# Optimization experiments

Measured on AMD Instinct MI355X. Metric: run time of the kernel, lower is better.

Reference implementation:

```python
import jax, jax.numpy as jnp
import numpy as np

N_NODES = 10000
NEG_SLOPE = 0.2
EPS = 1e-16


def gat_layer(x, W, a_src, a_dst, bias, src, dst):
    # x: [N, Fin], W: [Fin, Fout], a_src/a_dst: [Fout], bias: [Fout]
    h = x @ W                                  # [N, Fout]
    al_s = h @ a_src                           # [N]
    al_d = h @ a_dst                           # [N]
    e = jax.nn.leaky_relu(al_s[src] + al_d[dst], NEG_SLOPE)   # [E]
    # segment softmax over edges grouped by destination node
    m = jax.ops.segment_max(e, dst, num_segments=N_NODES)     # [N]
    ex = jnp.exp(e - m[dst])
    s = jax.ops.segment_sum(ex, dst, num_segments=N_NODES)    # [N]
    alpha = ex / (s[dst] + EPS)                                # [E]
    out = jax.ops.segment_sum(h[src] * alpha[:, None], dst, num_segments=N_NODES)
    return out + bias


def add_self_loops(edge_index):
    loop = jnp.arange(N_NODES, dtype=edge_index.dtype)
    return jnp.concatenate([edge_index, jnp.stack([loop, loop])], axis=1)


def setup_inputs() -> dict:
    key = jax.random.key(0)
    ks = jax.random.split(key, 12)
    F_in, F_hid, F_out = 256, 256, 256
    x = jax.random.normal(ks[0], (N_NODES, F_in), dtype=jnp.float32)
    pos_edge_index = jax.random.randint(ks[1], (2, 320000), 0, N_NODES)
    edge_index = jax.random.randint(ks[2], (2, 100000), 0, N_NODES)
    sc = lambda f: 1.0 / np.sqrt(f)
    Win_W = jax.random.normal(ks[3], (F_in, F_in), dtype=jnp.float32) * sc(F_in)
    Win_b = jnp.zeros((F_in,), dtype=jnp.float32)
    W1 = jax.random.normal(ks[4], (F_in, F_hid), dtype=jnp.float32) * sc(F_in)
    a1_src = jax.random.normal(ks[5], (F_hid,), dtype=jnp.float32) * sc(F_hid)
    a1_dst = jax.random.normal(ks[6], (F_hid,), dtype=jnp.float32) * sc(F_hid)
    b1 = jnp.zeros((F_hid,), dtype=jnp.float32)
    W2 = jax.random.normal(ks[7], (F_hid, F_out), dtype=jnp.float32) * sc(F_hid)
    a2_src = jax.random.normal(ks[8], (F_out,), dtype=jnp.float32) * sc(F_out)
    a2_dst = jax.random.normal(ks[9], (F_out,), dtype=jnp.float32) * sc(F_out)
    b2 = jnp.zeros((F_out,), dtype=jnp.float32)
    return {
        "x": x, "pos_edge_index": pos_edge_index, "edge_index": edge_index,
        "Win_W": Win_W, "Win_b": Win_b,
        "W1": W1, "a1_src": a1_src, "a1_dst": a1_dst, "b1": b1,
        "W2": W2, "a2_src": a2_src, "a2_dst": a2_dst, "b2": b2,
    }


def reference(x, pos_edge_index, edge_index, Win_W, Win_b,
              W1, a1_src, a1_dst, b1, W2, a2_src, a2_dst, b2):
    ei = add_self_loops(pos_edge_index)
    src, dst = ei[0], ei[1]
    h = x @ Win_W + Win_b                       # input_weighting Linear
    h = gat_layer(h, W1, a1_src, a1_dst, b1, src, dst)
    h = gat_layer(h, W2, a2_src, a2_dst, b2, src, dst)
    logits = jnp.sum(h[edge_index[0]] * h[edge_index[1]], axis=-1)
    return logits
```

## Files before the change

### kernel.cpp

```cpp
#include <hip/hip_runtime.h>
#include <math.h>

#define FDIM 256
#define NEG_SLOPE 0.2f

typedef _Float16 half4v __attribute__((ext_vector_type(4)));
typedef _Float16 half8v __attribute__((ext_vector_type(8)));
typedef float f32x4 __attribute__((ext_vector_type(4)));


__global__ void hist_dst(const int* __restrict__ pos_ei, int* __restrict__ cnt,
                         int E_pos, int E_tot) {
    int e = blockIdx.x * blockDim.x + threadIdx.x;
    if (e < E_tot) {
        int d = (e < E_pos) ? pos_ei[E_pos + e] : (e - E_pos);
        atomicAdd(&cnt[d], 1);
    }
}

__global__ __launch_bounds__(1024) void scan10k(const int* __restrict__ cnt,
                                                int* __restrict__ row_ptr,
                                                int* __restrict__ fill, int N) {
    const int CH = 10;
    __shared__ int sums[1024];
    int tid = threadIdx.x;
    int base = tid * CH;
    int vals[CH];
    int s = 0;
#pragma unroll
    for (int i = 0; i < CH; ++i) {
        int idx = base + i;
        int v = (idx < N) ? cnt[idx] : 0;
        vals[i] = s;
        s += v;
    }
    sums[tid] = s;
    __syncthreads();
    for (int off = 1; off < 1024; off <<= 1) {
        int v = (tid >= off) ? sums[tid - off] : 0;
        __syncthreads();
        sums[tid] += v;
        __syncthreads();
    }
    int toff = (tid == 0) ? 0 : sums[tid - 1];
#pragma unroll
    for (int i = 0; i < CH; ++i) {
        int idx = base + i;
        if (idx < N) {
            int rp = toff + vals[i];
            row_ptr[idx] = rp;
            fill[idx] = rp;
        }
    }
    if (tid == 0) row_ptr[N] = sums[1023];
}

__global__ void scatter_edges(const int* __restrict__ pos_ei, int* __restrict__ fill,
                              int* __restrict__ srcs, int E_pos, int E_tot) {
    int e = blockIdx.x * blockDim.x + threadIdx.x;
    if (e < E_tot) {
        int s, d;
        if (e < E_pos) { s = pos_ei[e]; d = pos_ei[E_pos + e]; }
        else           { s = e - E_pos; d = s; }
        int pos = atomicAdd(&fill[d], 1);
        srcs[pos] = s;
    }
}


__global__ __launch_bounds__(256) void prep_weights(const float* __restrict__ W0,
                                                    const float* __restrict__ W1,
                                                    const float* __restrict__ W2,
                                                    _Float16* __restrict__ Wt_hi,
                                                    _Float16* __restrict__ Wt_lo) {
    int n = blockIdx.x;
    int mat = blockIdx.y;
    const float* W = (mat == 0) ? W0 : (mat == 1) ? W1 : W2;
    int k = threadIdx.x;
    float v = W[k * FDIM + n];
    _Float16 hi = (_Float16)v;
    _Float16 lo = (_Float16)(v - (float)hi);
    size_t o = (size_t)mat * FDIM * FDIM + (size_t)n * FDIM + k;
    Wt_hi[o] = hi;
    Wt_lo[o] = lo;
}


template <int MODE>
__global__ __launch_bounds__(256) void gemm_mfma(
        const float* __restrict__ A32,
        const _Float16* __restrict__ A_hi, const _Float16* __restrict__ A_lo,
        const _Float16* __restrict__ Bt_hi, const _Float16* __restrict__ Bt_lo,
        const float* __restrict__ bias,
        const float* __restrict__ a_src, const float* __restrict__ a_dst,
        float* __restrict__ al_s, float* __restrict__ al_d,
        _Float16* __restrict__ C_hi, _Float16* __restrict__ C_lo,
        int M) {
    __shared__ _Float16 As_hi[64][72];
    __shared__ _Float16 As_lo[64][72];
    __shared__ _Float16 Bs_hi[64][72];
    __shared__ _Float16 Bs_lo[64][72];
    int tid = threadIdx.x;
    int lane = tid & 63, w = tid >> 6;
    int wm = w >> 1, wn = w & 1;
    int quad = lane >> 4, l16 = lane & 15;
    int mBase = blockIdx.x * 64, nBase = blockIdx.y * 64;
    f32x4 acc[2][2] = {};

    for (int k0 = 0; k0 < FDIM; k0 += 64) {
        __syncthreads();
        if (MODE == 0) {
#pragma unroll
            for (int i = 0; i < 4; ++i) {
                int f = tid + i * 256;
                int m = f >> 4, kc = (f & 15) << 2;
                int row = mBase + m;
                float4 a = make_float4(0.f, 0.f, 0.f, 0.f);
                if (row < M) a = *(const float4*)(A32 + (size_t)row * FDIM + k0 + kc);
                _Float16 hx = (_Float16)a.x, hy = (_Float16)a.y;
                _Float16 hz = (_Float16)a.z, hw = (_Float16)a.w;
                half4v hi = {hx, hy, hz, hw};
                half4v lo = {(_Float16)(a.x - (float)hx), (_Float16)(a.y - (float)hy),
                             (_Float16)(a.z - (float)hz), (_Float16)(a.w - (float)hw)};
                *(half4v*)&As_hi[m][kc] = hi;
                *(half4v*)&As_lo[m][kc] = lo;
            }
        } else {
#pragma unroll
            for (int i = 0; i < 2; ++i) {
                int g = tid + i * 256;
                int m = g >> 3, gk = (g & 7) << 3;
                int row = mBase + m;
                half8v hi, lo;
                if (row < M) {
                    size_t off = (size_t)row * FDIM + k0 + gk;
                    hi = *(const half8v*)(A_hi + off);
                    lo = *(const half8v*)(A_lo + off);
                } else {
                    _Float16 z = (_Float16)0.f;
                    hi = (half8v){z, z, z, z, z, z, z, z};
                    lo = hi;
                }
                *(half8v*)&As_hi[m][gk] = hi;
                *(half8v*)&As_lo[m][gk] = lo;
            }
        }
#pragma unroll
        for (int i = 0; i < 2; ++i) {
            int g = tid + i * 256;
            int n = g >> 3, gk = (g & 7) << 3;
            size_t off = (size_t)(nBase + n) * FDIM + k0 + gk;
            *(half8v*)&Bs_hi[n][gk] = *(const half8v*)(Bt_hi + off);
            *(half8v*)&Bs_lo[n][gk] = *(const half8v*)(Bt_lo + off);
        }
        __syncthreads();
#pragma unroll
        for (int ks = 0; ks < 2; ++ks) {
            int kcol = ks * 32 + quad * 8;
            half8v aHi[2], aLo[2], bHi[2], bLo[2];
#pragma unroll
            for (int mt = 0; mt < 2; ++mt) {
                int r = wm * 32 + mt * 16 + l16;
                aHi[mt] = *(const half8v*)&As_hi[r][kcol];
                aLo[mt] = *(const half8v*)&As_lo[r][kcol];
            }
#pragma unroll
            for (int nt = 0; nt < 2; ++nt) {
                int c = wn * 32 + nt * 16 + l16;
                bHi[nt] = *(const half8v*)&Bs_hi[c][kcol];
                bLo[nt] = *(const half8v*)&Bs_lo[c][kcol];
            }
#pragma unroll
            for (int mt = 0; mt < 2; ++mt)
#pragma unroll
                for (int nt = 0; nt < 2; ++nt) {
                    acc[mt][nt] = __builtin_amdgcn_mfma_f32_16x16x32_f16(
                        aHi[mt], bHi[nt], acc[mt][nt], 0, 0, 0);
                    acc[mt][nt] = __builtin_amdgcn_mfma_f32_16x16x32_f16(
                        aHi[mt], bLo[nt], acc[mt][nt], 0, 0, 0);
                    acc[mt][nt] = __builtin_amdgcn_mfma_f32_16x16x32_f16(
                        aLo[mt], bHi[nt], acc[mt][nt], 0, 0, 0);
                }
        }
    }

    int col0 = nBase + wn * 32 + l16;
    int col1 = col0 + 16;
    if (MODE == 0) {
        float b0 = bias[col0], b1v = bias[col1];
#pragma unroll
        for (int mt = 0; mt < 2; ++mt) {
#pragma unroll
            for (int r = 0; r < 4; ++r) {
                int row = mBase + wm * 32 + mt * 16 + quad * 4 + r;
                if (row >= M) continue;
                float o0 = acc[mt][0][r] + b0;
                float o1 = acc[mt][1][r] + b1v;
                _Float16 h0 = (_Float16)o0, h1 = (_Float16)o1;
                size_t p0 = (size_t)row * FDIM + col0;
                size_t p1 = (size_t)row * FDIM + col1;
                C_hi[p0] = h0;              C_hi[p1] = h1;
                C_lo[p0] = (_Float16)(o0 - (float)h0);
                C_lo[p1] = (_Float16)(o1 - (float)h1);
            }
        }
    } else {
        float as0 = a_src[col0], as1 = a_src[col1];
        float ad0 = a_dst[col0], ad1 = a_dst[col1];
#pragma unroll
        for (int mt = 0; mt < 2; ++mt) {
#pragma unroll
            for (int r = 0; r < 4; ++r) {
                int row = mBase + wm * 32 + mt * 16 + quad * 4 + r;
                if (row < M) {
                    C_hi[(size_t)row * FDIM + col0] = (_Float16)acc[mt][0][r];
                    C_hi[(size_t)row * FDIM + col1] = (_Float16)acc[mt][1][r];
                }
                float ps = acc[mt][0][r] * as0 + acc[mt][1][r] * as1;
                float pd = acc[mt][0][r] * ad0 + acc[mt][1][r] * ad1;
#pragma unroll
                for (int off = 8; off; off >>= 1) {
                    ps += __shfl_xor(ps, off);
                    pd += __shfl_xor(pd, off);
                }
                if (l16 == 0 && row < M) {
                    atomicAdd(&al_s[row], ps);
                    atomicAdd(&al_d[row], pd);
                }
            }
        }
    }
}


__global__ __launch_bounds__(256) void softagg(
        const _Float16* __restrict__ t, const float* __restrict__ al_s,
        const float* __restrict__ al_d, const int* __restrict__ row_ptr,
        const int* __restrict__ srcs, const float* __restrict__ bias,
        _Float16* __restrict__ out_hi, _Float16* __restrict__ out_lo,
        float* __restrict__ out32, int N) {
    int wave = threadIdx.x >> 6, lane = threadIdx.x & 63;
    int node = blockIdx.x * 4 + wave;
    if (node >= N) return;
    int beg = row_ptr[node], end = row_ptr[node + 1];
    int deg = end - beg;
    float ad = al_d[node];
    const _Float16* tb = t + (size_t)lane * 4;
    float4 acc = make_float4(0.f, 0.f, 0.f, 0.f);
    float ssum = 0.f;

    if (deg <= 256) {
        float e[4];
        int sj[4];
#pragma unroll
        for (int c = 0; c < 4; ++c) {
            e[c] = -INFINITY;
            sj[c] = 0;
            int j = beg + c * 64 + lane;
            if (j < end) {
                int s = srcs[j];
                sj[c] = s;
                float ee = al_s[s] + ad;
                e[c] = (ee > 0.f) ? ee : NEG_SLOPE * ee;
            }
        }
        float m = fmaxf(fmaxf(e[0], e[1]), fmaxf(e[2], e[3]));
#pragma unroll
        for (int o = 32; o; o >>= 1) m = fmaxf(m, __shfl_xor(m, o));
        float ex[4];
#pragma unroll
        for (int c = 0; c < 4; ++c) {
            ex[c] = (e[c] == -INFINITY) ? 0.f : __expf(e[c] - m);
            ssum += ex[c];
        }
#pragma unroll
        for (int c = 0; c < 4; ++c) {
            int jc = beg + c * 64;
            if (jc >= end) break;
            int cnt = min(64, end - jc);
            int jj = 0;
            for (; jj + 4 <= cnt; jj += 4) {
                float a0 = __shfl(ex[c], jj + 0), a1 = __shfl(ex[c], jj + 1);
                float a2 = __shfl(ex[c], jj + 2), a3 = __shfl(ex[c], jj + 3);
                int r0 = __shfl(sj[c], jj + 0), r1 = __shfl(sj[c], jj + 1);
                int r2 = __shfl(sj[c], jj + 2), r3 = __shfl(sj[c], jj + 3);
                half4v v0 = *(const half4v*)(tb + (size_t)r0 * FDIM);
                half4v v1 = *(const half4v*)(tb + (size_t)r1 * FDIM);
                half4v v2 = *(const half4v*)(tb + (size_t)r2 * FDIM);
                half4v v3 = *(const half4v*)(tb + (size_t)r3 * FDIM);
                acc.x = fmaf(a0, (float)v0.x, acc.x); acc.y = fmaf(a0, (float)v0.y, acc.y);
                acc.z = fmaf(a0, (float)v0.z, acc.z); acc.w = fmaf(a0, (float)v0.w, acc.w);
                acc.x = fmaf(a1, (float)v1.x, acc.x); acc.y = fmaf(a1, (float)v1.y, acc.y);
                acc.z = fmaf(a1, (float)v1.z, acc.z); acc.w = fmaf(a1, (float)v1.w, acc.w);
                acc.x = fmaf(a2, (float)v2.x, acc.x); acc.y = fmaf(a2, (float)v2.y, acc.y);
                acc.z = fmaf(a2, (float)v2.z, acc.z); acc.w = fmaf(a2, (float)v2.w, acc.w);
                acc.x = fmaf(a3, (float)v3.x, acc.x); acc.y = fmaf(a3, (float)v3.y, acc.y);
                acc.z = fmaf(a3, (float)v3.z, acc.z); acc.w = fmaf(a3, (float)v3.w, acc.w);
            }
            for (; jj < cnt; ++jj) {
                float a = __shfl(ex[c], jj);
                int r = __shfl(sj[c], jj);
                half4v v = *(const half4v*)(tb + (size_t)r * FDIM);
                acc.x = fmaf(a, (float)v.x, acc.x); acc.y = fmaf(a, (float)v.y, acc.y);
                acc.z = fmaf(a, (float)v.z, acc.z); acc.w = fmaf(a, (float)v.w, acc.w);
            }
        }
    } else {
        float m = -INFINITY;
        for (int j = beg + lane; j < end; j += 64) {
            float ee = al_s[srcs[j]] + ad;
            ee = (ee > 0.f) ? ee : NEG_SLOPE * ee;
            m = fmaxf(m, ee);
        }
#pragma unroll
        for (int o = 32; o; o >>= 1) m = fmaxf(m, __shfl_xor(m, o));
        for (int jc = beg; jc < end; jc += 64) {
            int j = jc + lane;
            float ex = 0.f;
            int sr = 0;
            if (j < end) {
                sr = srcs[j];
                float ee = al_s[sr] + ad;
                ee = (ee > 0.f) ? ee : NEG_SLOPE * ee;
                ex = __expf(ee - m);
                ssum += ex;
            }
            int cnt = min(64, end - jc);
            for (int jj = 0; jj < cnt; ++jj) {
                float a = __shfl(ex, jj);
                int r = __shfl(sr, jj);
                half4v v = *(const half4v*)(tb + (size_t)r * FDIM);
                acc.x = fmaf(a, (float)v.x, acc.x); acc.y = fmaf(a, (float)v.y, acc.y);
                acc.z = fmaf(a, (float)v.z, acc.z); acc.w = fmaf(a, (float)v.w, acc.w);
            }
        }
    }

#pragma unroll
    for (int o = 32; o; o >>= 1) ssum += __shfl_xor(ssum, o);
    float inv = 1.f / (ssum + 1e-16f);
    float4 bv = ((const float4*)bias)[lane];
    float ox = fmaf(acc.x, inv, bv.x);
    float oy = fmaf(acc.y, inv, bv.y);
    float oz = fmaf(acc.z, inv, bv.z);
    float ow = fmaf(acc.w, inv, bv.w);
    if (out32) {
        ((float4*)out32)[node * 64 + lane] = make_float4(ox, oy, oz, ow);
    } else {
        _Float16 hx = (_Float16)ox, hy = (_Float16)oy;
        _Float16 hz = (_Float16)oz, hw = (_Float16)ow;
        half4v hi = {hx, hy, hz, hw};
        half4v lo = {(_Float16)(ox - (float)hx), (_Float16)(oy - (float)hy),
                     (_Float16)(oz - (float)hz), (_Float16)(ow - (float)hw)};
        *(half4v*)(out_hi + (size_t)node * FDIM + lane * 4) = hi;
        *(half4v*)(out_lo + (size_t)node * FDIM + lane * 4) = lo;
    }
}


__global__ __launch_bounds__(256) void edge_dot(const float* __restrict__ h,
                                                const int* __restrict__ ei,
                                                float* __restrict__ out, int EQ) {
    int w = threadIdx.x >> 6, lane = threadIdx.x & 63;
    int e = blockIdx.x * 4 + w;
    if (e >= EQ) return;
    int u = ei[e], v = ei[EQ + e];
    const float4* hu = (const float4*)(h + (size_t)u * FDIM);
    const float4* hv = (const float4*)(h + (size_t)v * FDIM);
    float4 a = hu[lane], b = hv[lane];
    float s = a.x * b.x + a.y * b.y + a.z * b.z + a.w * b.w;
#pragma unroll
    for (int o = 32; o; o >>= 1) s += __shfl_down(s, o);
    if (lane == 0) out[e] = s;
}


extern "C" void kernel_launch(void* const* d_in, const int* in_sizes, int n_in,
                              void* d_out, int out_size, void* d_ws, size_t ws_size,
                              hipStream_t stream) {
    const float* x       = (const float*)d_in[0];
    const int*   pos_ei  = (const int*)d_in[1];
    const int*   q_ei    = (const int*)d_in[2];
    const float* Win_W   = (const float*)d_in[3];
    const float* Win_b   = (const float*)d_in[4];
    const float* W1      = (const float*)d_in[5];
    const float* a1_src  = (const float*)d_in[6];
    const float* a1_dst  = (const float*)d_in[7];
    const float* b1      = (const float*)d_in[8];
    const float* W2      = (const float*)d_in[9];
    const float* a2_src  = (const float*)d_in[10];
    const float* a2_dst  = (const float*)d_in[11];
    const float* b2      = (const float*)d_in[12];
    float* logits = (float*)d_out;

    const int N = in_sizes[0] / FDIM;
    const int E_pos = in_sizes[1] / 2;
    const int EQ = in_sizes[2] / 2;
    const int E_tot = E_pos + N;
    const size_t WMAT = (size_t)FDIM * FDIM;
    const size_t NF = (size_t)N * FDIM;

    _Float16* Wt_hi = (_Float16*)d_ws;
    _Float16* Wt_lo = Wt_hi + 3 * WMAT;
    _Float16* h0_hi = Wt_lo + 3 * WMAT;
    _Float16* h0_lo = h0_hi + NF;
    _Float16* t_h   = h0_lo + NF;
    float* h32   = (float*)(t_h + NF);
    float* al_s1 = h32 + NF;
    float* al_d1 = al_s1 + N;
    float* al_s2 = al_d1 + N;
    float* al_d2 = al_s2 + N;
    int* cnt     = (int*)(al_d2 + N);
    int* row_ptr = cnt + N;
    int* fill    = row_ptr + (N + 1);
    int* srcs    = fill + N;

    hipMemsetAsync(al_s1, 0, (size_t)(4 * N) * sizeof(float) + (size_t)N * sizeof(int), stream);

    {
        int nb = (E_tot + 255) / 256;
        hist_dst<<<nb, 256, 0, stream>>>(pos_ei, cnt, E_pos, E_tot);
        scan10k<<<1, 1024, 0, stream>>>(cnt, row_ptr, fill, N);
        scatter_edges<<<nb, 256, 0, stream>>>(pos_ei, fill, srcs, E_pos, E_tot);
    }

    prep_weights<<<dim3(FDIM, 3), 256, 0, stream>>>(Win_W, W1, W2, Wt_hi, Wt_lo);

    dim3 ggrid((N + 63) / 64, FDIM / 64);
    int nblk4 = (N + 3) / 4;

    gemm_mfma<0><<<ggrid, 256, 0, stream>>>(x, nullptr, nullptr, Wt_hi, Wt_lo, Win_b,
                                            nullptr, nullptr, nullptr, nullptr,
                                            h0_hi, h0_lo, N);

    gemm_mfma<1><<<ggrid, 256, 0, stream>>>(nullptr, h0_hi, h0_lo,
                                            Wt_hi + WMAT, Wt_lo + WMAT, nullptr,
                                            a1_src, a1_dst, al_s1, al_d1,
                                            t_h, nullptr, N);
    softagg<<<nblk4, 256, 0, stream>>>(t_h, al_s1, al_d1, row_ptr, srcs, b1,
                                       h0_hi, h0_lo, nullptr, N);

    gemm_mfma<1><<<ggrid, 256, 0, stream>>>(nullptr, h0_hi, h0_lo,
                                            Wt_hi + 2 * WMAT, Wt_lo + 2 * WMAT, nullptr,
                                            a2_src, a2_dst, al_s2, al_d2,
                                            t_h, nullptr, N);
    softagg<<<nblk4, 256, 0, stream>>>(t_h, al_s2, al_d2, row_ptr, srcs, b2,
                                       nullptr, nullptr, h32, N);

    edge_dot<<<(EQ + 3) / 4, 256, 0, stream>>>(h32, q_ei, logits, EQ);
}
```

Before: 239.3 us.

## Fuse graph-build kernels, batch softagg gathers by 8, group query edges by source

Merges the histogram and weight-prep kernels into one launch and the scatter into another, and adds a CSR build for the query edges keyed by source node. The final edge-dot kernel then walks each source's query edges so the source row is loaded once and reused. The softagg gather loops now issue 8 independent row loads per round instead of 4 or 1, to raise memory-level parallelism. The costs are an extra scan and scatter for the query CSR, and out-of-range shuffle lanes in partial rounds (their rows are still loaded but presumably weighted by zero).

```diff
diff --git a/kernel.cpp b/kernel.cpp
--- a/kernel.cpp
+++ b/kernel.cpp
@@ -9,20 +9,41 @@
 typedef float f32x4 __attribute__((ext_vector_type(4)));
 
 
-__global__ void hist_dst(const int* __restrict__ pos_ei, int* __restrict__ cnt,
-                         int E_pos, int E_tot) {
-    int e = blockIdx.x * blockDim.x + threadIdx.x;
-    if (e < E_tot) {
-        int d = (e < E_pos) ? pos_ei[E_pos + e] : (e - E_pos);
-        atomicAdd(&cnt[d], 1);
-    }
-}
-
-__global__ __launch_bounds__(1024) void scan10k(const int* __restrict__ cnt,
-                                                int* __restrict__ row_ptr,
-                                                int* __restrict__ fill, int N) {
+__global__ void build_phase1(const int* __restrict__ pos_ei, const int* __restrict__ q_ei,
+                             int* __restrict__ cnt, int* __restrict__ qcnt,
+                             const float* __restrict__ W0, const float* __restrict__ W1,
+                             const float* __restrict__ W2,
+                             _Float16* __restrict__ Wt_hi, _Float16* __restrict__ Wt_lo,
+                             int E_pos, int E_tot, int EQ, int nbE, int nbQ) {
+    int b = blockIdx.x;
+    int tid = threadIdx.x;
+    if (b < nbE) {
+        int e = b * 256 + tid;
+        if (e < E_tot) {
+            int d = (e < E_pos) ? pos_ei[E_pos + e] : (e - E_pos);
+            atomicAdd(&cnt[d], 1);
+        }
+    } else if (b < nbE + nbQ) {
+        int e = (b - nbE) * 256 + tid;
+        if (e < EQ) atomicAdd(&qcnt[q_ei[e]], 1);
+    } else {
+        int idx = b - nbE - nbQ;
+        int n = idx & 255, mat = idx >> 8;
+        const float* W = (mat == 0) ? W0 : (mat == 1) ? W1 : W2;
+        int k = tid;
+        float v = W[k * FDIM + n];
+        _Float16 hi = (_Float16)v;
+        _Float16 lo = (_Float16)(v - (float)hi);
+        size_t o = (size_t)mat * FDIM * FDIM + (size_t)n * FDIM + k;
+        Wt_hi[o] = hi;
+        Wt_lo[o] = lo;
+    }
+}
+
+
+__device__ void scan_body(const int* __restrict__ cnt, int* __restrict__ row_ptr,
+                          int* __restrict__ fill, int N, int* sums) {
     const int CH = 10;
-    __shared__ int sums[1024];
     int tid = threadIdx.x;
     int base = tid * CH;
     int vals[CH];
@@ -55,34 +76,43 @@
     if (tid == 0) row_ptr[N] = sums[1023];
 }
 
-__global__ void scatter_edges(const int* __restrict__ pos_ei, int* __restrict__ fill,
-                              int* __restrict__ srcs, int E_pos, int E_tot) {
-    int e = blockIdx.x * blockDim.x + threadIdx.x;
-    if (e < E_tot) {
-        int s, d;
-        if (e < E_pos) { s = pos_ei[e]; d = pos_ei[E_pos + e]; }
-        else           { s = e - E_pos; d = s; }
-        int pos = atomicAdd(&fill[d], 1);
-        srcs[pos] = s;
-    }
-}
-
-
-__global__ __launch_bounds__(256) void prep_weights(const float* __restrict__ W0,
-                                                    const float* __restrict__ W1,
-                                                    const float* __restrict__ W2,
-                                                    _Float16* __restrict__ Wt_hi,
-                                                    _Float16* __restrict__ Wt_lo) {
-    int n = blockIdx.x;
-    int mat = blockIdx.y;
-    const float* W = (mat == 0) ? W0 : (mat == 1) ? W1 : W2;
-    int k = threadIdx.x;
-    float v = W[k * FDIM + n];
-    _Float16 hi = (_Float16)v;
-    _Float16 lo = (_Float16)(v - (float)hi);
-    size_t o = (size_t)mat * FDIM * FDIM + (size_t)n * FDIM + k;
-    Wt_hi[o] = hi;
-    Wt_lo[o] = lo;
+__global__ __launch_bounds__(1024) void scan2(const int* __restrict__ cnt,
+                                              int* __restrict__ row_ptr, int* __restrict__ fill,
+                                              const int* __restrict__ qcnt,
+                                              int* __restrict__ qrow_ptr, int* __restrict__ qfill,
+                                              int N) {
+    __shared__ int sums[1024];
+    scan_body(cnt, row_ptr, fill, N, sums);
+    __syncthreads();
+    scan_body(qcnt, qrow_ptr, qfill, N, sums);
+}
+
+
+__global__ void build_phase2(const int* __restrict__ pos_ei, const int* __restrict__ q_ei,
+                             int* __restrict__ fill, int* __restrict__ srcs,
+                             int* __restrict__ qfill, int* __restrict__ qdst,
+                             int* __restrict__ qeid,
+                             int E_pos, int E_tot, int EQ, int nbE) {
+    int b = blockIdx.x;
+    int tid = threadIdx.x;
+    if (b < nbE) {
+        int e = b * 256 + tid;
+        if (e < E_tot) {
+            int s, d;
+            if (e < E_pos) { s = pos_ei[e]; d = pos_ei[E_pos + e]; }
+            else           { s = e - E_pos; d = s; }
+            int pos = atomicAdd(&fill[d], 1);
+            srcs[pos] = s;
+        }
+    } else {
+        int e = (b - nbE) * 256 + tid;
+        if (e < EQ) {
+            int u = q_ei[e];
+            int pos = atomicAdd(&qfill[u], 1);
+            qdst[pos] = q_ei[EQ + e];
+            qeid[pos] = e;
+        }
+    }
 }
 
 
@@ -278,31 +308,27 @@
             int jc = beg + c * 64;
             if (jc >= end) break;
             int cnt = min(64, end - jc);
-            int jj = 0;
-            for (; jj + 4 <= cnt; jj += 4) {
-                float a0 = __shfl(ex[c], jj + 0), a1 = __shfl(ex[c], jj + 1);
-                float a2 = __shfl(ex[c], jj + 2), a3 = __shfl(ex[c], jj + 3);
-                int r0 = __shfl(sj[c], jj + 0), r1 = __shfl(sj[c], jj + 1);
-                int r2 = __shfl(sj[c], jj + 2), r3 = __shfl(sj[c], jj + 3);
-                half4v v0 = *(const half4v*)(tb + (size_t)r0 * FDIM);
-                half4v v1 = *(const half4v*)(tb + (size_t)r1 * FDIM);
-                half4v v2 = *(const half4v*)(tb + (size_t)r2 * FDIM);
-                half4v v3 = *(const half4v*)(tb + (size_t)r3 * FDIM);
-                acc.x = fmaf(a0, (float)v0.x, acc.x); acc.y = fmaf(a0, (float)v0.y, acc.y);
-                acc.z = fmaf(a0, (float)v0.z, acc.z); acc.w = fmaf(a0, (float)v0.w, acc.w);
-                acc.x = fmaf(a1, (float)v1.x, acc.x); acc.y = fmaf(a1, (float)v1.y, acc.y);
-                acc.z = fmaf(a1, (float)v1.z, acc.z); acc.w = fmaf(a1, (float)v1.w, acc.w);
-                acc.x = fmaf(a2, (float)v2.x, acc.x); acc.y = fmaf(a2, (float)v2.y, acc.y);
-                acc.z = fmaf(a2, (float)v2.z, acc.z); acc.w = fmaf(a2, (float)v2.w, acc.w);
-                acc.x = fmaf(a3, (float)v3.x, acc.x); acc.y = fmaf(a3, (float)v3.y, acc.y);
-                acc.z = fmaf(a3, (float)v3.z, acc.z); acc.w = fmaf(a3, (float)v3.w, acc.w);
-            }
-            for (; jj < cnt; ++jj) {
-                float a = __shfl(ex[c], jj);
-                int r = __shfl(sj[c], jj);
-                half4v v = *(const half4v*)(tb + (size_t)r * FDIM);
-                acc.x = fmaf(a, (float)v.x, acc.x); acc.y = fmaf(a, (float)v.y, acc.y);
-                acc.z = fmaf(a, (float)v.z, acc.z); acc.w = fmaf(a, (float)v.w, acc.w);
+            int rounds = (cnt + 7) >> 3;
+            for (int g = 0; g < rounds; ++g) {
+                int jj = g * 8;
+                float av[8];
+                int rv[8];
+#pragma unroll
+                for (int q = 0; q < 8; ++q) {
+                    av[q] = __shfl(ex[c], jj + q);
+                    rv[q] = __shfl(sj[c], jj + q);
+                }
+                half4v vv[8];
+#pragma unroll
+                for (int q = 0; q < 8; ++q)
+                    vv[q] = *(const half4v*)(tb + (size_t)rv[q] * FDIM);
+#pragma unroll
+                for (int q = 0; q < 8; ++q) {
+                    acc.x = fmaf(av[q], (float)vv[q].x, acc.x);
+                    acc.y = fmaf(av[q], (float)vv[q].y, acc.y);
+                    acc.z = fmaf(av[q], (float)vv[q].z, acc.z);
+                    acc.w = fmaf(av[q], (float)vv[q].w, acc.w);
+                }
             }
         }
     } else {
@@ -326,12 +352,27 @@
                 ssum += ex;
             }
             int cnt = min(64, end - jc);
-            for (int jj = 0; jj < cnt; ++jj) {
-                float a = __shfl(ex, jj);
-                int r = __shfl(sr, jj);
-                half4v v = *(const half4v*)(tb + (size_t)r * FDIM);
-                acc.x = fmaf(a, (float)v.x, acc.x); acc.y = fmaf(a, (float)v.y, acc.y);
-                acc.z = fmaf(a, (float)v.z, acc.z); acc.w = fmaf(a, (float)v.w, acc.w);
+            int rounds = (cnt + 7) >> 3;
+            for (int g = 0; g < rounds; ++g) {
+                int jj = g * 8;
+                float av[8];
+                int rv[8];
+#pragma unroll
+                for (int q = 0; q < 8; ++q) {
+                    av[q] = __shfl(ex, jj + q);
+                    rv[q] = __shfl(sr, jj + q);
+                }
+                half4v vv[8];
+#pragma unroll
+                for (int q = 0; q < 8; ++q)
+                    vv[q] = *(const half4v*)(tb + (size_t)rv[q] * FDIM);
+#pragma unroll
+                for (int q = 0; q < 8; ++q) {
+                    acc.x = fmaf(av[q], (float)vv[q].x, acc.x);
+                    acc.y = fmaf(av[q], (float)vv[q].y, acc.y);
+                    acc.z = fmaf(av[q], (float)vv[q].z, acc.z);
+                    acc.w = fmaf(av[q], (float)vv[q].w, acc.w);
+                }
             }
         }
     }
@@ -358,20 +399,41 @@
 }
 
 
-__global__ __launch_bounds__(256) void edge_dot(const float* __restrict__ h,
-                                                const int* __restrict__ ei,
-                                                float* __restrict__ out, int EQ) {
+__global__ __launch_bounds__(256) void edge_dot_csr(
+        const float* __restrict__ h,
+        const int* __restrict__ qrow_ptr, const int* __restrict__ qdst,
+        const int* __restrict__ qeid, float* __restrict__ out, int N) {
     int w = threadIdx.x >> 6, lane = threadIdx.x & 63;
-    int e = blockIdx.x * 4 + w;
-    if (e >= EQ) return;
-    int u = ei[e], v = ei[EQ + e];
-    const float4* hu = (const float4*)(h + (size_t)u * FDIM);
-    const float4* hv = (const float4*)(h + (size_t)v * FDIM);
-    float4 a = hu[lane], b = hv[lane];
-    float s = a.x * b.x + a.y * b.y + a.z * b.z + a.w * b.w;
-#pragma unroll
-    for (int o = 32; o; o >>= 1) s += __shfl_down(s, o);
-    if (lane == 0) out[e] = s;
+    int u = blockIdx.x * 4 + w;
+    if (u >= N) return;
+    int beg = qrow_ptr[u], end = qrow_ptr[u + 1];
+    if (beg == end) return;
+    float4 a = ((const float4*)(h + (size_t)u * FDIM))[lane];
+    int j = beg;
+    for (; j + 2 <= end; j += 2) {
+        int v0 = qdst[j], v1 = qdst[j + 1];
+        float4 b0 = ((const float4*)(h + (size_t)v0 * FDIM))[lane];
+        float4 b1 = ((const float4*)(h + (size_t)v1 * FDIM))[lane];
+        float s0 = a.x * b0.x + a.y * b0.y + a.z * b0.z + a.w * b0.w;
+        float s1 = a.x * b1.x + a.y * b1.y + a.z * b1.z + a.w * b1.w;
+#pragma unroll
+        for (int o = 32; o; o >>= 1) {
+            s0 += __shfl_down(s0, o);
+            s1 += __shfl_down(s1, o);
+        }
+        if (lane == 0) {
+            out[qeid[j]] = s0;
+            out[qeid[j + 1]] = s1;
+        }
+    }
+    if (j < end) {
+        int v0 = qdst[j];
+        float4 b0 = ((const float4*)(h + (size_t)v0 * FDIM))[lane];
+        float s0 = a.x * b0.x + a.y * b0.y + a.z * b0.z + a.w * b0.w;
+#pragma unroll
+        for (int o = 32; o; o >>= 1) s0 += __shfl_down(s0, o);
+        if (lane == 0) out[qeid[j]] = s0;
+    }
 }
 
 
@@ -411,20 +473,26 @@
     float* al_s2 = al_d1 + N;
     float* al_d2 = al_s2 + N;
     int* cnt     = (int*)(al_d2 + N);
-    int* row_ptr = cnt + N;
+    int* qcnt    = cnt + N;
+    int* row_ptr = qcnt + N;
     int* fill    = row_ptr + (N + 1);
     int* srcs    = fill + N;
-
-    hipMemsetAsync(al_s1, 0, (size_t)(4 * N) * sizeof(float) + (size_t)N * sizeof(int), stream);
-
-    {
-        int nb = (E_tot + 255) / 256;
-        hist_dst<<<nb, 256, 0, stream>>>(pos_ei, cnt, E_pos, E_tot);
-        scan10k<<<1, 1024, 0, stream>>>(cnt, row_ptr, fill, N);
-        scatter_edges<<<nb, 256, 0, stream>>>(pos_ei, fill, srcs, E_pos, E_tot);
-    }
-
-    prep_weights<<<dim3(FDIM, 3), 256, 0, stream>>>(Win_W, W1, W2, Wt_hi, Wt_lo);
+    int* qrow_ptr= srcs + E_tot;
+    int* qfill   = qrow_ptr + (N + 1);
+    int* qdst    = qfill + N;
+    int* qeid    = qdst + EQ;
+
+    hipMemsetAsync(al_s1, 0, (size_t)(4 * N) * sizeof(float) + (size_t)(2 * N) * sizeof(int), stream);
+
+    int nbE = (E_tot + 255) / 256;
+    int nbQ = (EQ + 255) / 256;
+
+    build_phase1<<<nbE + nbQ + 768, 256, 0, stream>>>(pos_ei, q_ei, cnt, qcnt,
+                                                      Win_W, W1, W2, Wt_hi, Wt_lo,
+                                                      E_pos, E_tot, EQ, nbE, nbQ);
+    scan2<<<1, 1024, 0, stream>>>(cnt, row_ptr, fill, qcnt, qrow_ptr, qfill, N);
+    build_phase2<<<nbE + nbQ, 256, 0, stream>>>(pos_ei, q_ei, fill, srcs,
+                                                qfill, qdst, qeid, E_pos, E_tot, EQ, nbE);
 
     dim3 ggrid((N + 63) / 64, FDIM / 64);
     int nblk4 = (N + 3) / 4;
@@ -447,5 +515,5 @@
     softagg<<<nblk4, 256, 0, stream>>>(t_h, al_s2, al_d2, row_ptr, srcs, b2,
                                        nullptr, nullptr, h32, N);
 
-    edge_dot<<<(EQ + 3) / 4, 256, 0, stream>>>(h32, q_ei, logits, EQ);
-}
+    edge_dot_csr<<<nblk4, 256, 0, stream>>>(h32, qrow_ptr, qdst, qeid, logits, N);
+}
```

After: 252.5 us. +5.5%, slower.
